# Kernel optimization log

Measured on AMD Instinct MI355X. Metric: run time of the kernel, lower is better.

Reference implementation:

```python
import jax, jax.numpy as jnp
import numpy as np

T = 4096
HIDDEN = 2048
N_HEADS = 16
N_KV_HEADS = 4
HEAD_DIM = 128
WINDOW = 1024  # per_layer_sliding_window = WINDOW + 1 -> q attends keys with q_pos - k_pos <= WINDOW
ROPE_THETA = 100000.0
QKV_OUT = (N_HEADS + 2 * N_KV_HEADS) * HEAD_DIM  # 3072


def setup_inputs() -> dict:
    key = jax.random.key(0)
    k1, k2, k3, k4 = jax.random.split(key, 4)
    return {
        "hidden_states": jax.random.normal(k1, (T, HIDDEN), dtype=jnp.float32),
        "positions": jnp.arange(T, dtype=jnp.int32),
        "w_qkv": jax.random.normal(k2, (HIDDEN, QKV_OUT), dtype=jnp.float32) * 0.02,
        "b_qkv": jax.random.normal(k3, (QKV_OUT,), dtype=jnp.float32) * 0.02,
        "w_o": jax.random.normal(k4, (N_HEADS * HEAD_DIM, HIDDEN), dtype=jnp.float32) * 0.02,
    }


def _apply_rope(x, positions):
    # x: [T, n_heads, HEAD_DIM], neox-style rotary over full head dim
    half = HEAD_DIM // 2
    inv_freq = 1.0 / (ROPE_THETA ** (jnp.arange(half, dtype=jnp.float32) / half))
    freqs = positions.astype(jnp.float32)[:, None] * inv_freq[None, :]  # [T, half]
    cos = jnp.cos(freqs)[:, None, :]  # [T, 1, half]
    sin = jnp.sin(freqs)[:, None, :]
    x1, x2 = x[..., :half], x[..., half:]
    return jnp.concatenate([x1 * cos - x2 * sin, x2 * cos + x1 * sin], axis=-1)


def reference(hidden_states, positions, w_qkv, b_qkv, w_o):
    # QKV projection (bias=True)
    qkv = hidden_states @ w_qkv + b_qkv  # [T, QKV_OUT]
    q_size = N_HEADS * HEAD_DIM
    kv_size = N_KV_HEADS * HEAD_DIM
    q = qkv[:, :q_size].reshape(T, N_HEADS, HEAD_DIM)
    k = qkv[:, q_size:q_size + kv_size].reshape(T, N_KV_HEADS, HEAD_DIM)
    v = qkv[:, q_size + kv_size:].reshape(T, N_KV_HEADS, HEAD_DIM)

    # RoPE on q and k
    q = _apply_rope(q, positions)
    k = _apply_rope(k, positions)

    # GQA: expand kv heads to match query heads
    group = N_HEADS // N_KV_HEADS
    k = jnp.repeat(k, group, axis=1)  # [T, N_HEADS, HEAD_DIM]
    v = jnp.repeat(v, group, axis=1)

    scale = HEAD_DIM ** -0.5
    scores = jnp.einsum('qhd,khd->hqk', q, k) * scale  # [H, T, T]

    # causal + sliding-window mask: j <= i and i - j <= WINDOW
    i = jnp.arange(T)[:, None]
    j = jnp.arange(T)[None, :]
    mask = (j <= i) & (i - j <= WINDOW)  # [T, T]
    scores = jnp.where(mask[None, :, :], scores, jnp.finfo(scores.dtype).min)

    probs = jax.nn.softmax(scores, axis=-1)
    attn = jnp.einsum('hqk,khd->qhd', probs, v)  # [T, H, HEAD_DIM]
    attn = attn.reshape(T, N_HEADS * HEAD_DIM)

    # output projection (bias=False)
    return attn @ w_o
```

## Files before the change

### kernel.cpp

```cpp
#include <hip/hip_runtime.h>
#include <cstdint>

#define T_TOK 4096
#define HID 2048
#define NH 16
#define NKV 4
#define HD 128
#define WIN 1024
#define QKVO 3072

typedef float f32x4 __attribute__((ext_vector_type(4)));
typedef float f32x16 __attribute__((ext_vector_type(16)));
typedef __bf16 bf16x8 __attribute__((ext_vector_type(8)));
typedef __bf16 bf16x4 __attribute__((ext_vector_type(4)));
typedef unsigned int u32x4 __attribute__((ext_vector_type(4)));

__device__ __forceinline__ void gload16(const void* g, void* lds) {
  auto gp = reinterpret_cast<__attribute__((address_space(1))) void*>(
      reinterpret_cast<uintptr_t>(g));
  auto lp = reinterpret_cast<__attribute__((address_space(3))) void*>(
      reinterpret_cast<uintptr_t>(lds));
  __builtin_amdgcn_global_load_lds(gp, lp, 16, 0, 0);
}

__device__ __forceinline__ f32x4 mfma16(bf16x8 a, bf16x8 b, f32x4 c) {
  return __builtin_amdgcn_mfma_f32_16x16x32_bf16(a, b, c, 0, 0, 0);
}
__device__ __forceinline__ f32x16 mfma32(bf16x8 a, bf16x8 b, f32x16 c) {
  return __builtin_amdgcn_mfma_f32_32x32x16_bf16(a, b, c, 0, 0, 0);
}
__device__ __forceinline__ unsigned cvtpk(float lo, float hi) {
  unsigned r;
  asm("v_cvt_pk_bf16_f32 %0, %1, %2" : "=v"(r) : "v"(lo), "v"(hi));
  return r;
}
__device__ __forceinline__ void pl32swap(unsigned& a, unsigned& b) {
  asm volatile("v_permlane32_swap_b32 %0, %1" : "+v"(a), "+v"(b));
}

__global__ __launch_bounds__(256) void k_f32_to_bf16(const float* __restrict__ x,
                                                     __bf16* __restrict__ y) {
  const size_t e = (size_t)blockIdx.x * 256 + threadIdx.x;
  const float4* xv = (const float4*)x;
  float4 a = xv[e * 2], b = xv[e * 2 + 1];
  bf16x8 o;
  o[0] = (__bf16)a.x; o[1] = (__bf16)a.y; o[2] = (__bf16)a.z; o[3] = (__bf16)a.w;
  o[4] = (__bf16)b.x; o[5] = (__bf16)b.y; o[6] = (__bf16)b.z; o[7] = (__bf16)b.w;
  *(bf16x8*)(y + e * 8) = o;
}

__global__ __launch_bounds__(256) void k_transpose(const float* __restrict__ W,
                                                   __bf16* __restrict__ Wt,
                                                   int R, int C) {
  __shared__ __bf16 tb[32][33];
  const int nbx = C >> 5;
  const int c0 = (blockIdx.x % nbx) << 5;
  const int r0 = (blockIdx.x / nbx) << 5;
  const int tx = threadIdx.x & 31, ty = threadIdx.x >> 5;
#pragma unroll
  for (int i = 0; i < 32; i += 8)
    tb[ty + i][tx] = (__bf16)W[(size_t)(r0 + ty + i) * C + c0 + tx];
  __syncthreads();
#pragma unroll
  for (int i = 0; i < 32; i += 8)
    Wt[(size_t)(c0 + ty + i) * R + r0 + tx] = tb[tx][ty + i];
}

__global__ void k_rope_tab(const int* __restrict__ pos, float* __restrict__ cosT,
                           float* __restrict__ sinT) {
  const int t = blockIdx.x;
  const int d = threadIdx.x;
  const float inv = exp2f(-(float)d * (16.609640474436812f / 64.0f));
  const float fr = (float)pos[t] * inv;
  cosT[t * 64 + d] = cosf(fr);
  sinT[t * 64 + d] = sinf(fr);
}

template <bool BIAS, typename OutT>
__global__ __launch_bounds__(256, 2) void k_gemm(const __bf16* __restrict__ A,
                                                 const __bf16* __restrict__ Bt,
                                                 const float* __restrict__ bias,
                                                 OutT* __restrict__ C,
                                                 int M, int N, int K) {
  __shared__ __align__(16) __bf16 As[2][128 * 64];
  __shared__ __align__(16) __bf16 Bs[2][128 * 64];
  const int tid = threadIdx.x;
  const int lane = tid & 63;
  const int w = tid >> 6;
  const int wr = w >> 1, wc = w & 1;
  const int c = lane & 15, g = lane >> 4;
  const int csw = (c & 7) << 4;

  const int nstc = N >> 9;
  const int bid = blockIdx.x;
  const int xcd = bid & 7;
  const int j = bid >> 3;
  const int spx = (int)(gridDim.x >> 7);
  const int s = xcd * spx + (j >> 4);
  const int q = j & 15;
  const int by = (s / nstc) * 4 + (q >> 2);
  const int bx = (s % nstc) * 4 + (q & 3);
  const int m0 = by << 7, n0 = bx << 7;

  const int o0 = w * 4096 + lane * 16;
  const int srow = 32 * w + (lane >> 3);
  const int schunk = (lane & 7) ^ ((lane >> 3) & 7);
  const __bf16* gA0 = A + (size_t)(m0 + srow) * K + schunk * 8;
  const __bf16* gB0 = Bt + (size_t)(n0 + srow) * K + schunk * 8;

  f32x4 acc[4][4] = {};

  {
    char* la = (char*)&As[0][0];
    char* lb = (char*)&Bs[0][0];
#pragma unroll
    for (int qq = 0; qq < 4; qq++) {
      gload16(gA0 + (size_t)qq * 8 * K, la + o0 + qq * 1024);
      gload16(gB0 + (size_t)qq * 8 * K, lb + o0 + qq * 1024);
    }
  }
  __syncthreads();

  int cur = 0;
  for (int kt = 0; kt < K; kt += 64) {
    if (kt + 64 < K) {
      char* la = (char*)&As[0][0] + (cur ^ 1) * 16384;
      char* lb = (char*)&Bs[0][0] + (cur ^ 1) * 16384;
#pragma unroll
      for (int qq = 0; qq < 4; qq++) {
        gload16(gA0 + kt + 64 + (size_t)qq * 8 * K, la + o0 + qq * 1024);
        gload16(gB0 + kt + 64 + (size_t)qq * 8 * K, lb + o0 + qq * 1024);
      }
    }
    const char* as = (const char*)&As[0][0] + cur * 16384;
    const char* bs = (const char*)&Bs[0][0] + cur * 16384;
#pragma unroll
    for (int ds = 0; ds < 2; ds++) {
      bf16x8 af[4], bfr[4];
#pragma unroll
      for (int mi = 0; mi < 4; mi++)
        af[mi] = *(const bf16x8*)(as + (wr * 64 + mi * 16 + c) * 128 +
                                  ((ds * 64 + g * 16) ^ csw));
#pragma unroll
      for (int ni = 0; ni < 4; ni++)
        bfr[ni] = *(const bf16x8*)(bs + (wc * 64 + ni * 16 + c) * 128 +
                                   ((ds * 64 + g * 16) ^ csw));
#pragma unroll
      for (int mi = 0; mi < 4; mi++)
#pragma unroll
        for (int ni = 0; ni < 4; ni++)
          acc[mi][ni] = mfma16(af[mi], bfr[ni], acc[mi][ni]);
    }
    __syncthreads();
    cur ^= 1;
  }

#pragma unroll
  for (int ni = 0; ni < 4; ni++) {
    const int col = n0 + wc * 64 + ni * 16 + c;
    const float bv = BIAS ? bias[col] : 0.0f;
#pragma unroll
    for (int mi = 0; mi < 4; mi++)
#pragma unroll
      for (int r = 0; r < 4; r++) {
        const int row = m0 + wr * 64 + mi * 16 + 4 * g + r;
        C[(size_t)row * N + col] = (OutT)(acc[mi][ni][r] + bv);
      }
  }
}

__global__ __launch_bounds__(256) void k_rope_pack(
    const __bf16* __restrict__ qkv, const float* __restrict__ cosT,
    const float* __restrict__ sinT, __bf16* __restrict__ Qp,
    __bf16* __restrict__ Kp, __bf16* __restrict__ Vf) {
  const int t0 = blockIdx.x * 64;
  const int hh = blockIdx.y;
  const int tid = threadIdx.x;
  const int col0 = hh * HD;
  __shared__ __bf16 lt[64][136];
  if (hh < NH + NKV) {
    const bool isq = hh < NH;
    const float s = isq ? (0.08838834764831845f * 1.4426950408889634f) : 1.0f;
    __bf16* base = isq ? (Qp + (size_t)hh * T_TOK * HD)
                       : (Kp + (size_t)(hh - NH) * T_TOK * HD);
#pragma unroll
    for (int jj = 0; jj < 2; jj++) {
      const int e = jj * 256 + tid;
      const int tl = e >> 3, ch = e & 7;
      const int tt = t0 + tl;
      const bf16x8 x1 = *(const bf16x8*)(qkv + (size_t)tt * QKVO + col0 + ch * 8);
      const bf16x8 x2 = *(const bf16x8*)(qkv + (size_t)tt * QKVO + col0 + 64 + ch * 8);
      const float4 c0 = *(const float4*)(cosT + tt * 64 + ch * 8);
      const float4 c1 = *(const float4*)(cosT + tt * 64 + ch * 8 + 4);
      const float4 s0 = *(const float4*)(sinT + tt * 64 + ch * 8);
      const float4 s1 = *(const float4*)(sinT + tt * 64 + ch * 8 + 4);
      const float cs[8] = {c0.x, c0.y, c0.z, c0.w, c1.x, c1.y, c1.z, c1.w};
      const float sn[8] = {s0.x, s0.y, s0.z, s0.w, s1.x, s1.y, s1.z, s1.w};
      bf16x8 o1, o2;
#pragma unroll
      for (int i = 0; i < 8; i++) {
        const float a = (float)x1[i], b = (float)x2[i];
        o1[i] = (__bf16)((a * cs[i] - b * sn[i]) * s);
        o2[i] = (__bf16)((b * cs[i] + a * sn[i]) * s);
      }
      const int d2s = isq ? ch * 8 : ((ch * 8) ^ ((tt & 7) << 3));
      __bf16* dst = base + (size_t)tt * HD;
      *(bf16x8*)(dst + d2s) = o1;
      *(bf16x8*)(dst + 64 + d2s) = o2;
    }
  } else {
    const int kv = hh - (NH + NKV);
#pragma unroll
    for (int jj = 0; jj < 4; jj++) {
      const int e = jj * 256 + tid;
      const int tl = e >> 4, dc = e & 15;
      *(bf16x8*)&lt[tl][dc * 8] =
          *(const bf16x8*)(qkv + (size_t)(t0 + tl) * QKVO + col0 + dc * 8);
    }
    __syncthreads();
    __bf16* outb = Vf + ((size_t)kv * 64 + (t0 >> 6)) * 8192;
#pragma unroll
    for (int jj = 0; jj < 4; jj++) {
      const int u = jj * 256 + tid;
      const int lu = u & 63, ks = (u >> 6) & 3, m = u >> 8;
      const int d = m * 32 + (lu & 31);
      const int tb = ks * 16 + ((lu >> 5) << 3);
      bf16x8 o;
#pragma unroll
      for (int j = 0; j < 8; j++) o[j] = lt[tb + j][d];
      *(bf16x8*)(outb + (size_t)u * 8) = o;
    }
  }
}

__global__ __launch_bounds__(256, 2) void k_attn(const __bf16* __restrict__ Qp,
                                                 const __bf16* __restrict__ Kp,
                                                 const __bf16* __restrict__ Vf,
                                                 __bf16* __restrict__ attnO) {
  __shared__ __align__(16) __bf16 Ks[2][64 * 128];

  const int tid = threadIdx.x;
  const int lane = tid & 63;
  const int w = tid >> 6;
  const int l31 = lane & 31;
  const int hi = lane >> 5;
  const int swz = (lane & 7) << 4;
  const int h = blockIdx.y;
  const int kvh = h >> 2;
  const int qb = (int)(gridDim.x - 1) - (int)blockIdx.x;
  const int q0 = qb * 128;
  const int iw = q0 + 32 * w;
  const int irow = iw + l31;

  bf16x8 qf[8];
  {
    const __bf16* qbase = Qp + ((size_t)h * T_TOK + irow) * HD;
#pragma unroll
    for (int ds = 0; ds < 8; ds++)
      qf[ds] = *(const bf16x8*)(qbase + ds * 16 + hi * 8);
  }

  f32x16 ot[4] = {};
  float mrun = 0.0f, lrun = 0.0f;

  const int jstart = (q0 >= WIN) ? (q0 - WIN) : 0;
  const int niter = (q0 + 128 - jstart) >> 6;

  const char* Kg = (const char*)Kp + (size_t)kvh * T_TOK * HD * 2;
  const char* kg0 = Kg + (size_t)(jstart + 16 * w + (lane >> 4)) * 256 + (lane & 15) * 16;
  const __bf16* Vgb = Vf + (size_t)kvh * 64 * 8192;

#pragma unroll
  for (int q = 0; q < 4; q++)
    gload16(kg0 + q * 1024, (char*)&Ks[0][0] + w * 4096 + q * 1024);

  int cur = 0;

  for (int it = 0; it < niter; ++it) {
    const int j0 = jstart + it * 64;
    __syncthreads();

    if (it + 1 < niter) {
      const char* kg = kg0 + (size_t)(it + 1) * 16384;
      char* kd = (char*)&Ks[cur ^ 1][0] + w * 4096;
#pragma unroll
      for (int q = 0; q < 4; q++) gload16(kg + q * 1024, kd + q * 1024);
    }

    if (j0 > iw + 31) { cur ^= 1; continue; }
    if (iw - (j0 + 63) > WIN) { cur ^= 1; continue; }

    const __bf16* vt = Vgb + (size_t)(j0 >> 6) * 8192;
    bf16x8 vf[4][4];
#pragma unroll
    for (int m = 0; m < 4; m++)
#pragma unroll
      for (int ks = 0; ks < 4; ks++)
        vf[m][ks] = *(const bf16x8*)(vt + (m * 256 + ks * 64 + lane) * 8);

    const char* kb = (const char*)&Ks[cur][0];

    f32x16 st[2] = {};
    __builtin_amdgcn_s_setprio(1);
#pragma unroll
    for (int t = 0; t < 2; t++)
#pragma unroll
      for (int ds = 0; ds < 8; ds++) {
        bf16x8 kf = *(const bf16x8*)(kb + (t * 32 + l31) * 256 +
                                     ((ds * 32 + hi * 16) ^ swz));
        st[t] = mfma32(kf, qf[ds], st[t]);
      }
    __builtin_amdgcn_s_setprio(0);

    float p[2][16];
    float cmax = -1e30f;
    const bool interior = (j0 + 63 <= iw) && (iw + 31 - j0 <= WIN);
    if (interior) {
#pragma unroll
      for (int t = 0; t < 2; t++)
#pragma unroll
        for (int r = 0; r < 16; r++) {
          const float s = st[t][r];
          p[t][r] = s;
          cmax = fmaxf(cmax, s);
        }
    } else {
      const int jb = irow - j0 - 4 * hi;
#pragma unroll
      for (int t = 0; t < 2; t++)
#pragma unroll
        for (int r = 0; r < 16; r++) {
          float s = st[t][r];
          const int off = 32 * t + (r & 3) + 8 * (r >> 2);
          s = ((unsigned)(jb - off) <= WIN) ? s : -1e30f;
          p[t][r] = s;
          cmax = fmaxf(cmax, s);
        }
    }
    cmax = fmaxf(cmax, __shfl_xor(cmax, 32));

    if (!__all(cmax <= mrun + 11.54f)) {
      const float mn = fmaxf(mrun, cmax);
      const float alpha = exp2f(mrun - mn);
      lrun *= alpha;
#pragma unroll
      for (int m = 0; m < 4; m++) ot[m] *= alpha;
      mrun = mn;
    }
    float rs = 0.0f;
#pragma unroll
    for (int t = 0; t < 2; t++)
#pragma unroll
      for (int r = 0; r < 16; r++) {
        const float e_ = exp2f(p[t][r] - mrun);
        p[t][r] = e_;
        rs += e_;
      }
    rs += __shfl_xor(rs, 32);
    lrun += rs;

    bf16x8 pb[4];
#pragma unroll
    for (int t = 0; t < 2; t++) {
      unsigned wds[8];
#pragma unroll
      for (int i = 0; i < 8; i++) wds[i] = cvtpk(p[t][2 * i], p[t][2 * i + 1]);
      pl32swap(wds[0], wds[2]);
      pl32swap(wds[1], wds[3]);
      pl32swap(wds[4], wds[6]);
      pl32swap(wds[5], wds[7]);
      u32x4 f0 = {wds[0], wds[1], wds[2], wds[3]};
      u32x4 f1 = {wds[4], wds[5], wds[6], wds[7]};
      pb[2 * t] = __builtin_bit_cast(bf16x8, f0);
      pb[2 * t + 1] = __builtin_bit_cast(bf16x8, f1);
    }

    __builtin_amdgcn_s_setprio(1);
#pragma unroll
    for (int m = 0; m < 4; m++)
#pragma unroll
      for (int ks = 0; ks < 4; ks++)
        ot[m] = mfma32(vf[m][ks], pb[ks], ot[m]);
    __builtin_amdgcn_s_setprio(0);

    cur ^= 1;
  }

  const float inv_l = 1.0f / lrun;
  __bf16* orow = attnO + (size_t)irow * (NH * HD) + h * HD;
#pragma unroll
  for (int m = 0; m < 4; m++)
#pragma unroll
    for (int rg = 0; rg < 4; rg++) {
      const int d0 = 32 * m + 8 * rg + 4 * hi;
      bf16x4 o4;
#pragma unroll
      for (int r = 0; r < 4; r++) o4[r] = (__bf16)(ot[m][4 * rg + r] * inv_l);
      *(bf16x4*)(orow + d0) = o4;
    }
}

extern "C" void kernel_launch(void* const* d_in, const int* in_sizes, int n_in,
                              void* d_out, int out_size, void* d_ws, size_t ws_size,
                              hipStream_t stream) {
  (void)in_sizes; (void)n_in; (void)out_size; (void)ws_size;
  const float* hidden = (const float*)d_in[0];
  const int* positions = (const int*)d_in[1];
  const float* w_qkv = (const float*)d_in[2];
  const float* b_qkv = (const float*)d_in[3];
  const float* w_o = (const float*)d_in[4];
  float* out = (float*)d_out;

  char* ws = (char*)d_ws;
  __bf16* Hb = (__bf16*)ws;    ws += (size_t)T_TOK * HID * 2;
  __bf16* Wqkvt = (__bf16*)ws; ws += (size_t)QKVO * HID * 2;
  __bf16* Wot = (__bf16*)ws;   ws += (size_t)HID * HID * 2;
  float* cosT = (float*)ws;    ws += (size_t)T_TOK * 64 * 4;
  float* sinT = (float*)ws;    ws += (size_t)T_TOK * 64 * 4;
  __bf16* qkv = (__bf16*)ws;   ws += (size_t)T_TOK * QKVO * 2;
  __bf16* Qp = (__bf16*)ws;    ws += (size_t)NH * T_TOK * HD * 2;
  __bf16* Kp = (__bf16*)ws;    ws += (size_t)NKV * T_TOK * HD * 2;
  __bf16* Vfb = (__bf16*)ws;   ws += (size_t)NKV * 64 * 8192 * 2;
  __bf16* attnb = (__bf16*)ws; ws += (size_t)T_TOK * NH * HD * 2;

  k_f32_to_bf16<<<T_TOK * HID / (256 * 8), 256, 0, stream>>>(hidden, Hb);
  k_transpose<<<(QKVO / 32) * (HID / 32), 256, 0, stream>>>(w_qkv, Wqkvt, HID, QKVO);
  k_transpose<<<(HID / 32) * (HID / 32), 256, 0, stream>>>(w_o, Wot, HID, HID);
  k_rope_tab<<<T_TOK, 64, 0, stream>>>(positions, cosT, sinT);
  k_gemm<true, __bf16><<<(T_TOK / 128) * (QKVO / 128), 256, 0, stream>>>(
      Hb, Wqkvt, b_qkv, qkv, T_TOK, QKVO, HID);
  k_rope_pack<<<dim3(T_TOK / 64, NH + 2 * NKV), 256, 0, stream>>>(
      qkv, cosT, sinT, Qp, Kp, Vfb);
  k_attn<<<dim3(T_TOK / 128, NH), 256, 0, stream>>>(Qp, Kp, Vfb, attnb);
  k_gemm<false, float><<<(T_TOK / 128) * (HID / 128), 256, 0, stream>>>(
      attnb, Wot, nullptr, out, T_TOK, HID, HID);
}
```

Measured before the change: 183.5 us.

## Split attention KV range across two blocks and merge partials in combine kernel

Each query block's key range is split into two halves handled by separate workgroups (split-KV / flash-decoding style). Partial outputs plus running max and sum are written to workspace, and a new combine kernel rescales and merges them. Launch bounds also rise to 4 blocks per CU. The goal is more parallelism and occupancy (1024 blocks instead of 512), at the cost of an extra kernel launch, extra partial-output traffic and possible register spilling. The combine step assumes mrun is in log2 units, consistent with its use of exp2f.

```diff
diff --git a/kernel.cpp b/kernel.cpp
--- a/kernel.cpp
+++ b/kernel.cpp
@@ -233,10 +233,10 @@
   }
 }
 
-__global__ __launch_bounds__(256, 2) void k_attn(const __bf16* __restrict__ Qp,
-                                                 const __bf16* __restrict__ Kp,
-                                                 const __bf16* __restrict__ Vf,
-                                                 __bf16* __restrict__ attnO) {
+__global__ __launch_bounds__(256, 4) void k_attn(
+    const __bf16* __restrict__ Qp, const __bf16* __restrict__ Kp,
+    const __bf16* __restrict__ Vf, __bf16* __restrict__ Po,
+    float* __restrict__ Pl, float* __restrict__ Pm) {
   __shared__ __align__(16) __bf16 Ks[2][64 * 128];
 
   const int tid = threadIdx.x;
@@ -247,7 +247,8 @@
   const int swz = (lane & 7) << 4;
   const int h = blockIdx.y;
   const int kvh = h >> 2;
-  const int qb = (int)(gridDim.x - 1) - (int)blockIdx.x;
+  const int sb = (int)blockIdx.x & 1;
+  const int qb = 31 - ((int)blockIdx.x >> 1);
   const int q0 = qb * 128;
   const int iw = q0 + 32 * w;
   const int irow = iw + l31;
@@ -265,6 +266,9 @@
 
   const int jstart = (q0 >= WIN) ? (q0 - WIN) : 0;
   const int niter = (q0 + 128 - jstart) >> 6;
+  const int half = (niter + 1) >> 1;
+  const int it0 = sb ? half : 0;
+  const int it1 = sb ? niter : half;
 
   const char* Kg = (const char*)Kp + (size_t)kvh * T_TOK * HD * 2;
   const char* kg0 = Kg + (size_t)(jstart + 16 * w + (lane >> 4)) * 256 + (lane & 15) * 16;
@@ -272,15 +276,16 @@
 
 #pragma unroll
   for (int q = 0; q < 4; q++)
-    gload16(kg0 + q * 1024, (char*)&Ks[0][0] + w * 4096 + q * 1024);
+    gload16(kg0 + (size_t)it0 * 16384 + q * 1024,
+            (char*)&Ks[0][0] + w * 4096 + q * 1024);
 
   int cur = 0;
 
-  for (int it = 0; it < niter; ++it) {
+  for (int it = it0; it < it1; ++it) {
     const int j0 = jstart + it * 64;
     __syncthreads();
 
-    if (it + 1 < niter) {
+    if (it + 1 < it1) {
       const char* kg = kg0 + (size_t)(it + 1) * 16384;
       char* kd = (char*)&Ks[cur ^ 1][0] + w * 4096;
 #pragma unroll
@@ -386,8 +391,9 @@
     cur ^= 1;
   }
 
-  const float inv_l = 1.0f / lrun;
-  __bf16* orow = attnO + (size_t)irow * (NH * HD) + h * HD;
+  const float inv_l = (lrun > 0.0f) ? (1.0f / lrun) : 0.0f;
+  const size_t pblk = ((size_t)(h * 32 + qb)) * 2 + sb;
+  __bf16* prow = Po + pblk * 16384 + (size_t)(32 * w + l31) * 128;
 #pragma unroll
   for (int m = 0; m < 4; m++)
 #pragma unroll
@@ -396,8 +402,45 @@
       bf16x4 o4;
 #pragma unroll
       for (int r = 0; r < 4; r++) o4[r] = (__bf16)(ot[m][4 * rg + r] * inv_l);
-      *(bf16x4*)(orow + d0) = o4;
-    }
+      *(bf16x4*)(prow + d0) = o4;
+    }
+  if (hi == 0) {
+    const size_t ridx = pblk * 128 + 32 * w + l31;
+    Pl[ridx] = lrun;
+    Pm[ridx] = mrun;
+  }
+}
+
+__global__ __launch_bounds__(256) void k_combine(const __bf16* __restrict__ Po,
+                                                 const float* __restrict__ Pl,
+                                                 const float* __restrict__ Pm,
+                                                 __bf16* __restrict__ attnO) {
+  const int bid = blockIdx.x;
+  const int h = bid & 15, qb = bid >> 4;
+  const int tid = threadIdx.x;
+  const int r = tid >> 1;
+  const int dh = (tid & 1) * 64;
+  const size_t pb = ((size_t)(h * 32 + qb)) * 2;
+  const float m0 = Pm[pb * 128 + r], m1 = Pm[(pb + 1) * 128 + r];
+  const float l0 = Pl[pb * 128 + r], l1 = Pl[(pb + 1) * 128 + r];
+  const float M = fmaxf(m0, m1);
+  const float w0 = l0 * exp2f(m0 - M);
+  const float w1 = l1 * exp2f(m1 - M);
+  const float inv = 1.0f / (w0 + w1);
+  const float a0 = w0 * inv, a1 = w1 * inv;
+  const __bf16* p0 = Po + pb * 16384 + (size_t)r * 128 + dh;
+  const __bf16* p1 = Po + (pb + 1) * 16384 + (size_t)r * 128 + dh;
+  __bf16* od = attnO + (size_t)(qb * 128 + r) * (NH * HD) + h * HD + dh;
+#pragma unroll
+  for (int cc = 0; cc < 8; cc++) {
+    bf16x8 x0 = *(const bf16x8*)(p0 + cc * 8);
+    bf16x8 x1 = *(const bf16x8*)(p1 + cc * 8);
+    bf16x8 o;
+#pragma unroll
+    for (int j = 0; j < 8; j++)
+      o[j] = (__bf16)((float)x0[j] * a0 + (float)x1[j] * a1);
+    *(bf16x8*)(od + cc * 8) = o;
+  }
 }
 
 extern "C" void kernel_launch(void* const* d_in, const int* in_sizes, int n_in,
@@ -422,6 +465,9 @@
   __bf16* Kp = (__bf16*)ws;    ws += (size_t)NKV * T_TOK * HD * 2;
   __bf16* Vfb = (__bf16*)ws;   ws += (size_t)NKV * 64 * 8192 * 2;
   __bf16* attnb = (__bf16*)ws; ws += (size_t)T_TOK * NH * HD * 2;
+  __bf16* Po = (__bf16*)ws;    ws += (size_t)NH * 32 * 2 * 128 * 128 * 2;
+  float* Pl = (float*)ws;      ws += (size_t)NH * 32 * 2 * 128 * 4;
+  float* Pm = (float*)ws;      ws += (size_t)NH * 32 * 2 * 128 * 4;
 
   k_f32_to_bf16<<<T_TOK * HID / (256 * 8), 256, 0, stream>>>(hidden, Hb);
   k_transpose<<<(QKVO / 32) * (HID / 32), 256, 0, stream>>>(w_qkv, Wqkvt, HID, QKVO);
@@ -431,7 +477,8 @@
       Hb, Wqkvt, b_qkv, qkv, T_TOK, QKVO, HID);
   k_rope_pack<<<dim3(T_TOK / 64, NH + 2 * NKV), 256, 0, stream>>>(
       qkv, cosT, sinT, Qp, Kp, Vfb);
-  k_attn<<<dim3(T_TOK / 128, NH), 256, 0, stream>>>(Qp, Kp, Vfb, attnb);
+  k_attn<<<dim3(64, NH), 256, 0, stream>>>(Qp, Kp, Vfb, Po, Pl, Pm);
+  k_combine<<<512, 256, 0, stream>>>(Po, Pl, Pm, attnb);
   k_gemm<false, float><<<(T_TOK / 128) * (HID / 128), 256, 0, stream>>>(
       attnb, Wot, nullptr, out, T_TOK, HID, HID);
 }
```

Result: slower. 498.9 us (+171.9%).

## Merge weight transposes into one vectorized kernel and remap attention blocks to XCDs

Applied to the files above, without the earlier changes.

The two weight transpose launches become a single kernel that uses 64x64 tiles, float4 global loads and 16-byte bf16 stores, in place of 32x32 tiles with scalar accesses. Attention moves to a 1D grid whose block index is remapped so the four query heads sharing a KV head land on the same XCD pair, with heavy query blocks still scheduled first. The aim is fewer launches, wider memory transactions in the transpose, and better L2 reuse of K/V in attention. The transpose's LDS reads are strided and may hit bank conflicts, and the head mapping assumes blocks are dispatched round-robin across 8 XCDs.

```diff
diff --git a/kernel.cpp b/kernel.cpp
--- a/kernel.cpp
+++ b/kernel.cpp
@@ -49,21 +49,43 @@
   *(bf16x8*)(y + e * 8) = o;
 }
 
-__global__ __launch_bounds__(256) void k_transpose(const float* __restrict__ W,
-                                                   __bf16* __restrict__ Wt,
-                                                   int R, int C) {
-  __shared__ __bf16 tb[32][33];
-  const int nbx = C >> 5;
-  const int c0 = (blockIdx.x % nbx) << 5;
-  const int r0 = (blockIdx.x / nbx) << 5;
-  const int tx = threadIdx.x & 31, ty = threadIdx.x >> 5;
-#pragma unroll
-  for (int i = 0; i < 32; i += 8)
-    tb[ty + i][tx] = (__bf16)W[(size_t)(r0 + ty + i) * C + c0 + tx];
+__global__ __launch_bounds__(256) void k_transpose2(
+    const float* __restrict__ W1, __bf16* __restrict__ Wt1,
+    const float* __restrict__ W2, __bf16* __restrict__ Wt2) {
+  __shared__ float lt[64][69];
+  int bid = blockIdx.x;
+  const float* W;
+  __bf16* Wt;
+  int R, C;
+  if (bid < 1536) {
+    W = W1; Wt = Wt1; R = HID; C = QKVO;
+  } else {
+    bid -= 1536; W = W2; Wt = Wt2; R = HID; C = HID;
+  }
+  const int nbx = C >> 6;
+  const int c0 = (bid % nbx) << 6;
+  const int r0 = (bid / nbx) << 6;
+  const int tid = threadIdx.x;
+  const int tx = tid & 15, ty = tid >> 4;
+#pragma unroll
+  for (int i = 0; i < 4; i++) {
+    const int r = ty + 16 * i;
+    const float4 v = *(const float4*)(W + (size_t)(r0 + r) * C + c0 + 4 * tx);
+    lt[r][4 * tx] = v.x;
+    lt[r][4 * tx + 1] = v.y;
+    lt[r][4 * tx + 2] = v.z;
+    lt[r][4 * tx + 3] = v.w;
+  }
   __syncthreads();
-#pragma unroll
-  for (int i = 0; i < 32; i += 8)
-    Wt[(size_t)(c0 + ty + i) * R + r0 + tx] = tb[tx][ty + i];
+  const int ux = tid & 7, uy = tid >> 3;
+#pragma unroll
+  for (int i = 0; i < 2; i++) {
+    const int c = uy + 32 * i;
+    bf16x8 o;
+#pragma unroll
+    for (int k = 0; k < 8; k++) o[k] = (__bf16)lt[8 * ux + k][c];
+    *(bf16x8*)(Wt + (size_t)(c0 + c) * R + r0 + 8 * ux) = o;
+  }
 }
 
 __global__ void k_rope_tab(const int* __restrict__ pos, float* __restrict__ cosT,
@@ -245,9 +267,11 @@
   const int l31 = lane & 31;
   const int hi = lane >> 5;
   const int swz = (lane & 7) << 4;
-  const int h = blockIdx.y;
+  const int bid = blockIdx.x;
+  const int xcd = bid & 7, j = bid >> 3;
+  const int h = ((xcd >> 1) << 2) + ((xcd & 1) << 1) + (j & 1);
+  const int qb = 31 - (j >> 1);
   const int kvh = h >> 2;
-  const int qb = (int)(gridDim.x - 1) - (int)blockIdx.x;
   const int q0 = qb * 128;
   const int iw = q0 + 32 * w;
   const int irow = iw + l31;
@@ -424,14 +448,13 @@
   __bf16* attnb = (__bf16*)ws; ws += (size_t)T_TOK * NH * HD * 2;
 
   k_f32_to_bf16<<<T_TOK * HID / (256 * 8), 256, 0, stream>>>(hidden, Hb);
-  k_transpose<<<(QKVO / 32) * (HID / 32), 256, 0, stream>>>(w_qkv, Wqkvt, HID, QKVO);
-  k_transpose<<<(HID / 32) * (HID / 32), 256, 0, stream>>>(w_o, Wot, HID, HID);
+  k_transpose2<<<2560, 256, 0, stream>>>(w_qkv, Wqkvt, w_o, Wot);
   k_rope_tab<<<T_TOK, 64, 0, stream>>>(positions, cosT, sinT);
   k_gemm<true, __bf16><<<(T_TOK / 128) * (QKVO / 128), 256, 0, stream>>>(
       Hb, Wqkvt, b_qkv, qkv, T_TOK, QKVO, HID);
   k_rope_pack<<<dim3(T_TOK / 64, NH + 2 * NKV), 256, 0, stream>>>(
       qkv, cosT, sinT, Qp, Kp, Vfb);
-  k_attn<<<dim3(T_TOK / 128, NH), 256, 0, stream>>>(Qp, Kp, Vfb, attnb);
+  k_attn<<<512, 256, 0, stream>>>(Qp, Kp, Vfb, attnb);
   k_gemm<false, float><<<(T_TOK / 128) * (HID / 128), 256, 0, stream>>>(
       attnb, Wot, nullptr, out, T_TOK, HID, HID);
 }
```

After: 178.5 us. 2.7% less time.
